# Performance work log

Measured on AMD Instinct MI355X. Metric: run time of the kernel, lower is better.

## Reference

```python
import jax, jax.numpy as jnp
import numpy as np

B, S, D = 32, 512, 512          # batch, max splits, HIDDEN_SIZE
H2 = D // 2                      # bidirectional GRU hidden per direction = 256
HEADS = 8
ATT_H = 512                      # ML_ATT_HIDDEN
DK = ATT_H // HEADS
LN_EPS = 1e-5


def setup_inputs() -> dict:
    key = jax.random.key(0)
    ks = jax.random.split(key, 20)
    n = lambda k, shp, s=0.05: jax.random.normal(k, shp, dtype=jnp.float32) * s
    lengths = jax.random.randint(ks[0], (B,), 1, S + 1)
    masks = (jnp.arange(S)[None, :] < lengths[:, None]).astype(jnp.int32)
    return {
        "splits": n(ks[1], (B, S, D), 1.0),
        "w_ih_f": n(ks[2], (3 * H2, D)), "w_hh_f": n(ks[3], (3 * H2, H2)),
        "b_ih_f": n(ks[4], (3 * H2,)), "b_hh_f": n(ks[5], (3 * H2,)),
        "w_ih_b": n(ks[6], (3 * H2, D)), "w_hh_b": n(ks[7], (3 * H2, H2)),
        "b_ih_b": n(ks[8], (3 * H2,)), "b_hh_b": n(ks[9], (3 * H2,)),
        "ln1_g": jnp.ones((D,), jnp.float32), "ln1_b": jnp.zeros((D,), jnp.float32),
        "wq": n(ks[10], (ATT_H, D)), "bq": n(ks[11], (ATT_H,)),
        "wk": n(ks[12], (ATT_H, D)), "bk": n(ks[13], (ATT_H,)),
        "wv": n(ks[14], (ATT_H, D)), "bv": n(ks[15], (ATT_H,)),
        "wo": n(ks[16], (D, ATT_H)), "bo": n(ks[17], (D,)),
        "ln2_g": jnp.ones((D,), jnp.float32), "ln2_b": jnp.zeros((D,), jnp.float32),
        "lengths": lengths, "masks": masks,
    }


def _gru_dir(x, m, w_ih, w_hh, b_ih, b_hh):
    """x: (B,S,D) float, m: (B,S) float {0,1}. Masked GRU, packed-sequence semantics:
    hidden frozen past length, outputs zero at pads, returns (outputs (B,S,H2), h_final (B,H2))."""
    xg = jnp.einsum('bsd,gd->bsg', x, w_ih) + b_ih   # precompute input gates (B,S,3H2)
    xg_t = xg.transpose(1, 0, 2)                      # (S,B,3H2)
    m_t = m.T[:, :, None]                             # (S,B,1)
    h0 = jnp.zeros((x.shape[0], w_hh.shape[1]), x.dtype)

    def step(h, inp):
        xg_s, m_s = inp
        hg = h @ w_hh.T + b_hh
        xr, xz, xn = jnp.split(xg_s, 3, -1)
        hr, hz, hn = jnp.split(hg, 3, -1)
        r = jax.nn.sigmoid(xr + hr)
        z = jax.nn.sigmoid(xz + hz)
        ncand = jnp.tanh(xn + r * hn)
        h_new = (1.0 - z) * ncand + z * h
        h = m_s * h_new + (1.0 - m_s) * h
        return h, h * m_s

    hT, ys = jax.lax.scan(step, h0, (xg_t, m_t))
    return ys.transpose(1, 0, 2), hT


def _layernorm(x, g, b):
    mu = x.mean(-1, keepdims=True)
    var = ((x - mu) ** 2).mean(-1, keepdims=True)
    return (x - mu) / jnp.sqrt(var + LN_EPS) * g + b


def reference(splits, w_ih_f, w_hh_f, b_ih_f, b_hh_f, w_ih_b, w_hh_b, b_ih_b, b_hh_b,
              ln1_g, ln1_b, wq, bq, wk, bk, wv, bv, wo, bo, ln2_g, ln2_b,
              lengths, masks):
    mf = masks.astype(splits.dtype)  # (B,S)
    # bidirectional masked GRU (split_rnn)
    out_f, h_f = _gru_dir(splits, mf, w_ih_f, w_hh_f, b_ih_f, b_hh_f)
    out_b_rev, h_b = _gru_dir(splits[:, ::-1], mf[:, ::-1], w_ih_b, w_hh_b, b_ih_b, b_hh_b)
    outputs = jnp.concatenate([out_f, out_b_rev[:, ::-1]], -1)  # (B,S,D)
    hidden = jnp.concatenate([h_f, h_b], -1)                    # (B,D)
    zm = (lengths != 0).astype(outputs.dtype)
    outputs = outputs * zm[:, None, None]
    hidden = hidden * zm[:, None]
    # split_rnn_norm (LAYER_NORM_USE)
    outputs = _layernorm(outputs, ln1_g, ln1_b)
    # CONTEXT_ATT: masked multi-head self-attention
    m3 = mf[:, None, :] * mf[:, :, None]        # (B,S,S)
    bsz = outputs.shape[0]

    def proj(x, w, b):
        return (x @ w.T + b).reshape(bsz, -1, HEADS, DK).transpose(0, 2, 1, 3)

    q = proj(outputs, wq, bq)
    k = proj(outputs, wk, bk)
    v = proj(outputs, wv, bv)
    scores = jnp.einsum('bhqd,bhkd->bhqk', q, k) / np.sqrt(DK).astype(outputs.dtype)
    mask4 = m3[:, None, :, :]
    scores = jnp.where(mask4 == 0, jnp.asarray(-1e8, scores.dtype), scores)
    p = jax.nn.softmax(scores, axis=-1) * mask4
    attn = jnp.einsum('bhqk,bhkd->bhqd', p, v)
    concat = attn.transpose(0, 2, 1, 3).reshape(bsz, -1, HEADS * DK)
    o = concat @ wo.T + bo
    rowmask = (m3.sum(-1, keepdims=True) > 0).astype(o.dtype)   # (B,S,1)
    o = o * rowmask
    # residual + attn_norm
    outputs = _layernorm(outputs + o, ln2_g, ln2_b)
    return outputs, hidden
```

## Files before the change

kernel.cpp:

```cpp
#include <hip/hip_runtime.h>
#include <hip/hip_bf16.h>
#include <hip/hip_fp16.h>


typedef __bf16 bf16_t;
typedef _Float16 f16_t;
typedef __bf16 bf16x8 __attribute__((ext_vector_type(8)));
typedef __bf16 bf16x4 __attribute__((ext_vector_type(4)));
typedef _Float16 f16x8 __attribute__((ext_vector_type(8)));
typedef float f32x4 __attribute__((ext_vector_type(4)));

#define NB 32
#define NS 512
#define ND 512
#define NH 8
#define DKq 64
#define CH 32

static __device__ __forceinline__ float sigm(float x){ return 1.0f/(1.0f+__expf(-x)); }
static __device__ __forceinline__ float tanh_fast(float x){ return 1.0f - 2.0f/(__expf(2.0f*x)+1.0f); }

__global__ void cvt_f32_bf16_k(const float* __restrict__ src, bf16_t* __restrict__ dst, int n4){
    int i = blockIdx.x*256 + threadIdx.x;
    if (i < n4){
        float4 v = ((const float4*)src)[i];
        bf16x4 o; o[0]=(bf16_t)v.x; o[1]=(bf16_t)v.y; o[2]=(bf16_t)v.z; o[3]=(bf16_t)v.w;
        ((bf16x4*)dst)[i] = o;
    }
}

struct CvtSeg { const float* src; bf16_t* dst; int n4; };
struct CvtArgs { CvtSeg seg[6]; };
__global__ void cvt_multi_k(CvtArgs a){
    CvtSeg s = a.seg[blockIdx.y];
    int i = blockIdx.x*256 + threadIdx.x;
    if (i < s.n4){
        float4 v = ((const float4*)s.src)[i];
        bf16x4 o; o[0]=(bf16_t)v.x; o[1]=(bf16_t)v.y; o[2]=(bf16_t)v.z; o[3]=(bf16_t)v.w;
        ((bf16x4*)s.dst)[i] = o;
    }
}

template<int MODE>
__global__ __launch_bounds__(256,2) void gemm_k(
    const bf16_t* __restrict__ A, const bf16_t* __restrict__ W,
    const float* __restrict__ bias, void* __restrict__ out, void* __restrict__ out2,
    const int* __restrict__ masks, int N)
{
    const int lane = threadIdx.x & 63;
    const int wv = threadIdx.x >> 6;
    const int wr = wv >> 1, wc = wv & 1;
    const int nx = gridDim.x;
    int lin = blockIdx.y * nx + blockIdx.x;
    int xcd = lin & 7, idx = lin >> 3;
    int yl = idx / nx, xb = idx - yl*nx;
    int yb = xcd*16 + yl;
    const int m0 = yb*128 + wr*64;
    const int n0 = xb*128 + wc*64;
    const int r16 = lane & 15, kq = lane >> 4;
    f32x4 acc[4][4] = {};
    const bf16_t* Ap = A + (size_t)(m0 + r16)*512 + kq*8;
    const bf16_t* Wp = W + (size_t)(n0 + r16)*512 + kq*8;
    #pragma unroll
    for (int kk = 0; kk < 16; ++kk){
        bf16x8 a[4], b[4];
        #pragma unroll
        for (int i=0;i<4;++i) a[i] = *(const bf16x8*)(Ap + (size_t)i*16*512 + kk*32);
        #pragma unroll
        for (int j=0;j<4;++j) b[j] = *(const bf16x8*)(Wp + (size_t)j*16*512 + kk*32);
        #pragma unroll
        for (int i=0;i<4;++i)
            #pragma unroll
            for (int j=0;j<4;++j)
                acc[i][j] = __builtin_amdgcn_mfma_f32_16x16x32_bf16(a[i], b[j], acc[i][j], 0,0,0);
    }
    #pragma unroll
    for (int i=0;i<4;++i){
        int row_base = m0 + i*16 + kq*4;
        #pragma unroll
        for (int j=0;j<4;++j){
            int col = n0 + j*16 + r16;
            float bs = bias[col];
            #pragma unroll
            for (int r=0;r<4;++r){
                int row = row_base + r;
                float v = acc[i][j][r] + bs;
                if (MODE==0){
                    if (col < 768) ((f16_t*)out)[(size_t)row*768 + col] = (f16_t)v;
                    else           ((f16_t*)out2)[(size_t)row*768 + (col-768)] = (f16_t)v;
                } else if (MODE==1){
                    int which = col >> 9, hh = (col >> 6) & 7, d = col & 63;
                    int bb = row >> 9, s = row & 511;
                    ((bf16_t*)out)[((((size_t)which*NB + bb)*NH + hh)*NS + s)*DKq + d] = (bf16_t)v;
                } else {
                    float mrow = (float)masks[row];
                    ((float*)out)[(size_t)row*N + col] = v * mrow;
                }
            }
        }
    }
}

__global__ __launch_bounds__(512,2) void gru_scan_k(
    const f16_t* __restrict__ xg_f, const f16_t* __restrict__ xg_b,
    const float* __restrict__ whh_f, const float* __restrict__ whh_b,
    const float* __restrict__ bhh_f, const float* __restrict__ bhh_b,
    const int* __restrict__ lengths,
    f16_t* __restrict__ gout,
    float* __restrict__ hidden)
{
    const int b = blockIdx.x >> 1, dir = blockIdx.x & 1;
    const int tid = threadIdx.x, lane = tid & 63, w = tid >> 6;
    const int r16 = lane & 15, kq = lane >> 4;
    const float* whh = dir ? whh_b : whh_f;
    const float* bhh = dir ? bhh_b : bhh_f;
    const f16_t* xgd = dir ? xg_b : xg_f;
    const int len = lengths[b];

    __shared__ __align__(16) f16_t  xg_lds[2][CH][768];
    __shared__ __align__(16) bf16_t h_row[2][256];

    ((bf16_t*)h_row)[tid & 511] = (bf16_t)0.0f;

    const int t0 = dir ? (NS - len) : 0;
    const int t_end = dir ? NS : len;
    const int nch = (len + CH - 1) / CH;

    auto issue_chunk = [&](int ci, int buf){
        int base = t0 + ci*CH;
        int jmax = min(CH, t_end - base);
        int pstart = dir ? (NS - base - jmax) : base;
        const char* gp = (const char*)(xgd + ((size_t)b*NS + pstart)*768);
        char* lp = (char*)(&xg_lds[buf][0][0]);
        int bytes = jmax*1536;
        #pragma unroll
        for (int k2=0; k2<6; ++k2){
            int off = (w*6 + k2)*1024;
            if (off < bytes){
                __builtin_amdgcn_global_load_lds(
                    (const __attribute__((address_space(1))) void*)(gp + off + (size_t)lane*16),
                    (__attribute__((address_space(3))) void*)(lp + off), 16, 0, 0);
            }
        }
    };
    issue_chunk(0, 0);

    bf16x8 wf[6][8];
    #pragma unroll
    for (int tt=0; tt<6; ++tt){
        int g = tt >> 1, u = tt & 1;
        int n0 = g*256 + 32*w + u*16;
        const float* wp = whh + (size_t)(n0 + r16)*256 + kq*8;
        #pragma unroll
        for (int kk=0; kk<8; ++kk){
            float4 v0 = *(const float4*)(wp + kk*32);
            float4 v1 = *(const float4*)(wp + kk*32 + 4);
            bf16x8 f;
            f[0]=(bf16_t)v0.x; f[1]=(bf16_t)v0.y; f[2]=(bf16_t)v0.z; f[3]=(bf16_t)v0.w;
            f[4]=(bf16_t)v1.x; f[5]=(bf16_t)v1.y; f[6]=(bf16_t)v1.z; f[7]=(bf16_t)v1.w;
            wf[tt][kk] = f;
        }
    }
    float bhr[2], bhz[2], bhn[2], hreg[2];
    #pragma unroll
    for (int u=0; u<2; ++u){
        int gi = 32*w + 16*u + r16;
        bhr[u] = bhh[gi]; bhz[u] = bhh[256+gi]; bhn[u] = bhh[512+gi];
        hreg[u] = 0.0f;
    }

    int hp = 0;
    for (int ci = 0; ci < nch; ++ci){
        const int cur = ci & 1;
        const int base = t0 + ci*CH;
        const int jmax = min(CH, t_end - base);
        __syncthreads();
        if (ci + 1 < nch) issue_chunk(ci+1, cur^1);
        for (int j = 0; j < jmax; ++j){
            const int xrow = dir ? (jmax-1-j) : j;
            float xr[2], xz[2], xn[2];
            if (lane < 16){
                #pragma unroll
                for (int u=0; u<2; ++u){
                    int gi = 32*w + 16*u + r16;
                    xr[u] = (float)xg_lds[cur][xrow][gi];
                    xz[u] = (float)xg_lds[cur][xrow][256+gi];
                    xn[u] = (float)xg_lds[cur][xrow][512+gi];
                }
            }
            f32x4 acc[6] = {};
            #pragma unroll
            for (int kk=0; kk<8; ++kk){
                bf16x8 a = {};
                if (r16 == 0) a = *(const bf16x8*)(&h_row[hp][kk*32 + kq*8]);
                #pragma unroll
                for (int tt=0; tt<6; ++tt)
                    acc[tt] = __builtin_amdgcn_mfma_f32_16x16x32_bf16(a, wf[tt][kk], acc[tt], 0,0,0);
            }
            if (lane < 16){
                int t = base + j;
                int pos = dir ? (NS-1-t) : t;
                #pragma unroll
                for (int u=0; u<2; ++u){
                    int gi = 32*w + 16*u + r16;
                    float hr = acc[u][0]   + bhr[u];
                    float hz = acc[2+u][0] + bhz[u];
                    float hn = acc[4+u][0] + bhn[u];
                    float rr = sigm(xr[u] + hr);
                    float z2 = sigm(xz[u] + hz);
                    float nc = tanh_fast(xn[u] + rr*hn);
                    hreg[u] = (1.0f - z2)*nc + z2*hreg[u];
                    h_row[hp^1][gi] = (bf16_t)hreg[u];
                    gout[((size_t)b*NS + pos)*512 + dir*256 + gi] = (f16_t)hreg[u];
                }
            }
            hp ^= 1;
            asm volatile("s_waitcnt lgkmcnt(0)" ::: "memory");
            __builtin_amdgcn_s_barrier();
            asm volatile("" ::: "memory");
        }
    }
    if (lane < 16){
        #pragma unroll
        for (int u=0; u<2; ++u)
            hidden[(size_t)b*512 + dir*256 + 32*w + 16*u + r16] = hreg[u];
    }
}

template<int PASS>
__global__ __launch_bounds__(256,4) void ln_k(
    const void* __restrict__ src1, const float* __restrict__ src2,
    const float* __restrict__ gg, const float* __restrict__ bb,
    void* __restrict__ dst)
{
    int row = blockIdx.x*4 + (threadIdx.x>>6);
    int lane = threadIdx.x & 63;
    int c0 = lane*8;
    float x[8];
    if (PASS==1){
        f16x8 v = *(const f16x8*)((const f16_t*)src1 + (size_t)row*512 + c0);
        #pragma unroll
        for (int i=0;i<8;++i) x[i] = (float)v[i];
    } else {
        bf16x8 v = *(const bf16x8*)((const bf16_t*)src1 + (size_t)row*512 + c0);
        const float* q = src2 + (size_t)row*512 + c0;
        float4 q0 = *(const float4*)q, q1 = *(const float4*)(q+4);
        x[0]=(float)v[0]+q0.x; x[1]=(float)v[1]+q0.y; x[2]=(float)v[2]+q0.z; x[3]=(float)v[3]+q0.w;
        x[4]=(float)v[4]+q1.x; x[5]=(float)v[5]+q1.y; x[6]=(float)v[6]+q1.z; x[7]=(float)v[7]+q1.w;
    }
    float s=0.f, sq=0.f;
    #pragma unroll
    for (int i=0;i<8;++i){ s += x[i]; sq += x[i]*x[i]; }
    #pragma unroll
    for (int m=1; m<64; m<<=1){ s += __shfl_xor(s, m, 64); sq += __shfl_xor(sq, m, 64); }
    float mu = s * (1.0f/512.0f);
    float var = sq * (1.0f/512.0f) - mu*mu;
    float rs = rsqrtf(var + 1e-5f);
    if (PASS==1){
        bf16x8 o;
        #pragma unroll
        for (int i=0;i<8;++i) o[i] = (bf16_t)((x[i]-mu)*rs*gg[c0+i] + bb[c0+i]);
        *(bf16x8*)((bf16_t*)dst + (size_t)row*512 + c0) = o;
    } else {
        float y[8];
        #pragma unroll
        for (int i=0;i<8;++i) y[i] = (x[i]-mu)*rs*gg[c0+i] + bb[c0+i];
        float* dp = (float*)dst + (size_t)row*512 + c0;
        *(float4*)dp     = make_float4(y[0],y[1],y[2],y[3]);
        *(float4*)(dp+4) = make_float4(y[4],y[5],y[6],y[7]);
    }
}

__global__ __launch_bounds__(256,2) void attn_k(
    const bf16_t* __restrict__ qkv,
    const int* __restrict__ lengths,
    bf16_t* __restrict__ concat)
{
    int lin = blockIdx.x + 8*(blockIdx.y + 8*blockIdx.z);
    int xcd = lin & 7, idx = lin >> 3;
    int qb = idx & 7;
    int bh = (xcd << 5) | (idx >> 3);
    int hh = bh & 7, b = bh >> 3;
    const int tid = threadIdx.x, lane = tid & 63, w = tid >> 6;
    const int r16 = lane & 15, kq = lane >> 4;
    const int len = lengths[b];
    const size_t bhof = ((size_t)b*NH + hh)*NS*DKq;
    const bf16_t* Q = qkv + bhof;
    const bf16_t* K = qkv + (size_t)NB*NH*NS*DKq + bhof;
    const bf16_t* V = qkv + 2*(size_t)NB*NH*NS*DKq + bhof;

    __shared__ __align__(16) bf16_t VT[32][520];
    __shared__ __align__(16) bf16_t P[4][16][40];

    const int q0 = qb*64 + w*16;
    bf16x8 aq[2];
    #pragma unroll
    for (int kk=0; kk<2; ++kk)
        aq[kk] = *(const bf16x8*)(Q + (size_t)(q0+r16)*DKq + kk*32 + kq*8);

    f32x4 sc[32] = {};
    #pragma unroll
    for (int t=0;t<32;++t){
        #pragma unroll
        for (int kk=0;kk<2;++kk){
            bf16x8 bk = *(const bf16x8*)(K + (size_t)(t*16+r16)*DKq + kk*32 + kq*8);
            sc[t] = __builtin_amdgcn_mfma_f32_16x16x32_bf16(aq[kk], bk, sc[t], 0,0,0);
        }
    }
    float mx[4] = {-3e38f,-3e38f,-3e38f,-3e38f};
    #pragma unroll
    for (int t=0;t<32;++t){
        bool valid = (t*16 + r16) < len;
        #pragma unroll
        for (int r=0;r<4;++r){
            float sv = valid ? sc[t][r]*0.125f : -3e38f;
            sc[t][r] = sv;
            mx[r] = fmaxf(mx[r], sv);
        }
    }
    #pragma unroll
    for (int m=1;m<16;m<<=1)
        #pragma unroll
        for (int r=0;r<4;++r) mx[r] = fmaxf(mx[r], __shfl_xor(mx[r], m, 64));
    float sm[4] = {0.f,0.f,0.f,0.f};
    #pragma unroll
    for (int t=0;t<32;++t){
        bool valid = (t*16 + r16) < len;
        #pragma unroll
        for (int r=0;r<4;++r){
            float p = valid ? __expf(sc[t][r] - mx[r]) : 0.0f;
            sc[t][r] = p;
            sm[r] += p;
        }
    }
    #pragma unroll
    for (int m=1;m<16;m<<=1)
        #pragma unroll
        for (int r=0;r<4;++r) sm[r] += __shfl_xor(sm[r], m, 64);
    float rs[4];
    #pragma unroll
    for (int r=0;r<4;++r) rs[r] = sm[r] > 0.f ? 1.0f/sm[r] : 0.0f;

    f32x4 ao[4] = {};
    #pragma unroll
    for (int half=0; half<2; ++half){
        __syncthreads();
        #pragma unroll
        for (int rr=0; rr<2; ++rr){
            int s = tid*2 + rr;
            const bf16_t* vp = V + (size_t)s*DKq + half*32;
            bf16x8 v0 = *(const bf16x8*)(vp);
            bf16x8 v1 = *(const bf16x8*)(vp+8);
            bf16x8 v2 = *(const bf16x8*)(vp+16);
            bf16x8 v3 = *(const bf16x8*)(vp+24);
            #pragma unroll
            for (int d=0; d<8; ++d){
                VT[d][s]=v0[d]; VT[8+d][s]=v1[d]; VT[16+d][s]=v2[d]; VT[24+d][s]=v3[d];
            }
        }
        __syncthreads();
        #pragma unroll
        for (int c=0;c<16;++c){
            #pragma unroll
            for (int tt=0;tt<2;++tt)
                #pragma unroll
                for (int r=0;r<4;++r)
                    P[w][kq*4 + r][tt*16 + r16] = (bf16_t)(sc[2*c+tt][r] * rs[r]);
            bf16x8 pa = *(const bf16x8*)(&P[w][r16][kq*8]);
            #pragma unroll
            for (int jt=0;jt<2;++jt){
                bf16x8 bvv = *(const bf16x8*)(&VT[jt*16 + r16][c*32 + kq*8]);
                ao[half*2+jt] = __builtin_amdgcn_mfma_f32_16x16x32_bf16(pa, bvv, ao[half*2+jt], 0,0,0);
            }
        }
    }
    #pragma unroll
    for (int ht=0; ht<4; ++ht){
        int d = (ht>>1)*32 + ((ht&1)*16) + r16;
        #pragma unroll
        for (int r=0;r<4;++r){
            int s = q0 + kq*4 + r;
            float v = (s < len) ? ao[ht][r] : 0.0f;
            concat[((size_t)b*NS + s)*512 + hh*DKq + d] = (bf16_t)v;
        }
    }
}

extern "C" void kernel_launch(void* const* d_in, const int* in_sizes, int n_in,
                              void* d_out, int out_size, void* d_ws, size_t ws_size,
                              hipStream_t stream){
    (void)in_sizes; (void)n_in; (void)out_size; (void)ws_size;
    const float* splits = (const float*)d_in[0];
    const float* w_ih_f = (const float*)d_in[1];
    const float* w_hh_f = (const float*)d_in[2];
    const float* b_ih_f = (const float*)d_in[3];
    const float* b_hh_f = (const float*)d_in[4];
    const float* w_ih_b = (const float*)d_in[5];
    const float* w_hh_b = (const float*)d_in[6];
    const float* b_ih_b = (const float*)d_in[7];
    const float* b_hh_b = (const float*)d_in[8];
    const float* ln1_g  = (const float*)d_in[9];
    const float* ln1_b  = (const float*)d_in[10];
    const float* wq     = (const float*)d_in[11];
    const float* bq     = (const float*)d_in[12];
    const float* wk     = (const float*)d_in[13];
    const float* bk_    = (const float*)d_in[14];
    const float* wv     = (const float*)d_in[15];
    const float* bv     = (const float*)d_in[16];
    const float* wo     = (const float*)d_in[17];
    const float* bo     = (const float*)d_in[18];
    const float* ln2_g  = (const float*)d_in[19];
    const float* ln2_b  = (const float*)d_in[20];
    const int* lengths  = (const int*)d_in[21];
    const int* masks    = (const int*)d_in[22];

    char* ws = (char*)d_ws;
    bf16_t* splits16 = (bf16_t*)(ws);
    f16_t*  xg_f     = (f16_t*)(ws + ((size_t)16<<20));
    f16_t*  xg_b     = (f16_t*)(ws + ((size_t)40<<20));
    f16_t*  gout     = (f16_t*)(ws + ((size_t)64<<20));
    bf16_t* ln1out   = (bf16_t*)(ws + ((size_t)80<<20));
    bf16_t* wih16    = (bf16_t*)(ws + ((size_t)96<<20));
    bf16_t* wqkv16   = (bf16_t*)(ws + ((size_t)98<<20));
    bf16_t* wo16     = (bf16_t*)(ws + ((size_t)100<<20));
    float*  bih      = (float*)(ws + ((size_t)101<<20));
    float*  bqkv     = (float*)(ws + ((size_t)101<<20) + 8192);
    bf16_t* qkv      = (bf16_t*)xg_f;
    float*  obuf     = (float*)xg_f;
    bf16_t* concat   = (bf16_t*)splits16;

    float* out_f = (float*)d_out;
    float* hid   = out_f + (size_t)NB*NS*ND;

    hipLaunchKernelGGL(cvt_f32_bf16_k, dim3(8192), dim3(256), 0, stream, splits, splits16, 2097152);
    CvtArgs ca;
    ca.seg[0] = { w_ih_f, wih16,          98304 };
    ca.seg[1] = { w_ih_b, wih16+393216,   98304 };
    ca.seg[2] = { wq,     wqkv16,         65536 };
    ca.seg[3] = { wk,     wqkv16+262144,  65536 };
    ca.seg[4] = { wv,     wqkv16+524288,  65536 };
    ca.seg[5] = { wo,     wo16,           65536 };
    hipLaunchKernelGGL(cvt_multi_k, dim3(384,6), dim3(256), 0, stream, ca);
    hipMemcpyAsync(bih,       b_ih_f, 768*4, hipMemcpyDeviceToDevice, stream);
    hipMemcpyAsync(bih+768,   b_ih_b, 768*4, hipMemcpyDeviceToDevice, stream);
    hipMemcpyAsync(bqkv,      bq,     512*4, hipMemcpyDeviceToDevice, stream);
    hipMemcpyAsync(bqkv+512,  bk_,    512*4, hipMemcpyDeviceToDevice, stream);
    hipMemcpyAsync(bqkv+1024, bv,     512*4, hipMemcpyDeviceToDevice, stream);
    hipMemsetAsync(gout, 0, (size_t)16<<20, stream);

    hipLaunchKernelGGL((gemm_k<0>), dim3(12,128), dim3(256), 0, stream,
                       splits16, wih16, bih, (void*)xg_f, (void*)xg_b, nullptr, 1536);
    hipLaunchKernelGGL(gru_scan_k, dim3(64), dim3(512), 0, stream,
                       xg_f, xg_b, w_hh_f, w_hh_b, b_hh_f, b_hh_b, lengths, gout, hid);
    hipLaunchKernelGGL((ln_k<1>), dim3(4096), dim3(256), 0, stream,
                       (const void*)gout, nullptr, ln1_g, ln1_b, (void*)ln1out);
    hipLaunchKernelGGL((gemm_k<1>), dim3(12,128), dim3(256), 0, stream,
                       ln1out, wqkv16, bqkv, (void*)qkv, nullptr, nullptr, 0);
    hipLaunchKernelGGL(attn_k, dim3(8,8,32), dim3(256), 0, stream, qkv, lengths, concat);
    hipLaunchKernelGGL((gemm_k<2>), dim3(4,128), dim3(256), 0, stream,
                       concat, wo16, bo, (void*)obuf, nullptr, masks, 512);
    hipLaunchKernelGGL((ln_k<2>), dim3(4096), dim3(256), 0, stream,
                       (const void*)ln1out, obuf, ln2_g, ln2_b, (void*)out_f);
}
```

Baseline: 1.249 ms.

## Replace GRU recurrent MFMA with fp16 dot2 across 1024 threads, batch output stores

The GRU scan kernel drops the MFMA matvec, which wasted most of its lanes because only one row of the A operand was non-zero. In its place, each of 1024 threads computes partial dot products with packed fp16 fdot2 on register-resident weights, and the partials are reduced with cross-lane shuffles. Hidden outputs are staged in LDS per chunk and written to global memory as coalesced vector stores, and the chunk size is halved to fit the larger block. The recurrent weights and hidden state change from bf16 to fp16, and the per-step barrier becomes a full __syncthreads across 16 waves, which may cost more synchronization per step.

Result: slower. 1.298 ms (+3.9%).

```diff
diff --git a/kernel.cpp b/kernel.cpp
--- a/kernel.cpp
+++ b/kernel.cpp
@@ -8,6 +8,8 @@
 typedef __bf16 bf16x8 __attribute__((ext_vector_type(8)));
 typedef __bf16 bf16x4 __attribute__((ext_vector_type(4)));
 typedef _Float16 f16x8 __attribute__((ext_vector_type(8)));
+typedef _Float16 f16x4 __attribute__((ext_vector_type(4)));
+typedef _Float16 f16x2 __attribute__((ext_vector_type(2)));
 typedef float f32x4 __attribute__((ext_vector_type(4)));
 
 #define NB 32
@@ -15,7 +17,7 @@
 #define ND 512
 #define NH 8
 #define DKq 64
-#define CH 32
+#define CH 16
 
 static __device__ __forceinline__ float sigm(float x){ return 1.0f/(1.0f+__expf(-x)); }
 static __device__ __forceinline__ float tanh_fast(float x){ return 1.0f - 2.0f/(__expf(2.0f*x)+1.0f); }
@@ -101,7 +103,7 @@
     }
 }
 
-__global__ __launch_bounds__(512,2) void gru_scan_k(
+__global__ __launch_bounds__(1024,4) void gru_scan_k(
     const f16_t* __restrict__ xg_f, const f16_t* __restrict__ xg_b,
     const float* __restrict__ whh_f, const float* __restrict__ whh_b,
     const float* __restrict__ bhh_f, const float* __restrict__ bhh_b,
@@ -112,15 +114,17 @@
     const int b = blockIdx.x >> 1, dir = blockIdx.x & 1;
     const int tid = threadIdx.x, lane = tid & 63, w = tid >> 6;
     const int r16 = lane & 15, kq = lane >> 4;
+    const int c = (w << 4) | r16;
     const float* whh = dir ? whh_b : whh_f;
     const float* bhh = dir ? bhh_b : bhh_f;
     const f16_t* xgd = dir ? xg_b : xg_f;
     const int len = lengths[b];
 
-    __shared__ __align__(16) f16_t  xg_lds[2][CH][768];
-    __shared__ __align__(16) bf16_t h_row[2][256];
-
-    ((bf16_t*)h_row)[tid & 511] = (bf16_t)0.0f;
+    __shared__ __align__(16) f16_t xg_lds[2][CH][768];
+    __shared__ __align__(16) f16_t go_lds[CH][256];
+    __shared__ __align__(16) f16_t h_row[2][256];
+
+    if (tid < 512) ((f16_t*)h_row)[tid] = (f16_t)0.0f;
 
     const int t0 = dir ? (NS - len) : 0;
     const int t_end = dir ? NS : len;
@@ -134,40 +138,33 @@
         char* lp = (char*)(&xg_lds[buf][0][0]);
         int bytes = jmax*1536;
         #pragma unroll
-        for (int k2=0; k2<6; ++k2){
-            int off = (w*6 + k2)*1024;
-            if (off < bytes){
+        for (int k2=0; k2<2; ++k2){
+            int woff = (k2*16 + w)*1024;
+            if (woff < bytes){
                 __builtin_amdgcn_global_load_lds(
-                    (const __attribute__((address_space(1))) void*)(gp + off + (size_t)lane*16),
-                    (__attribute__((address_space(3))) void*)(lp + off), 16, 0, 0);
+                    (const __attribute__((address_space(1))) void*)(gp + woff + (size_t)lane*16),
+                    (__attribute__((address_space(3))) void*)(lp + woff), 16, 0, 0);
             }
         }
     };
     issue_chunk(0, 0);
 
-    bf16x8 wf[6][8];
-    #pragma unroll
-    for (int tt=0; tt<6; ++tt){
-        int g = tt >> 1, u = tt & 1;
-        int n0 = g*256 + 32*w + u*16;
-        const float* wp = whh + (size_t)(n0 + r16)*256 + kq*8;
+    f16x2 wd[3][8][4];
+    #pragma unroll
+    for (int g=0; g<3; ++g){
+        const float* wp = whh + (size_t)(g*256 + c)*256 + kq*8;
         #pragma unroll
         for (int kk=0; kk<8; ++kk){
             float4 v0 = *(const float4*)(wp + kk*32);
             float4 v1 = *(const float4*)(wp + kk*32 + 4);
-            bf16x8 f;
-            f[0]=(bf16_t)v0.x; f[1]=(bf16_t)v0.y; f[2]=(bf16_t)v0.z; f[3]=(bf16_t)v0.w;
-            f[4]=(bf16_t)v1.x; f[5]=(bf16_t)v1.y; f[6]=(bf16_t)v1.z; f[7]=(bf16_t)v1.w;
-            wf[tt][kk] = f;
-        }
-    }
-    float bhr[2], bhz[2], bhn[2], hreg[2];
-    #pragma unroll
-    for (int u=0; u<2; ++u){
-        int gi = 32*w + 16*u + r16;
-        bhr[u] = bhh[gi]; bhz[u] = bhh[256+gi]; bhn[u] = bhh[512+gi];
-        hreg[u] = 0.0f;
-    }
+            wd[g][kk][0] = (f16x2){(f16_t)v0.x, (f16_t)v0.y};
+            wd[g][kk][1] = (f16x2){(f16_t)v0.z, (f16_t)v0.w};
+            wd[g][kk][2] = (f16x2){(f16_t)v1.x, (f16_t)v1.y};
+            wd[g][kk][3] = (f16x2){(f16_t)v1.z, (f16_t)v1.w};
+        }
+    }
+    const float bhr = bhh[c], bhz = bhh[256+c], bhn = bhh[512+c];
+    float hreg = 0.0f;
 
     int hp = 0;
     for (int ci = 0; ci < nch; ++ci){
@@ -178,53 +175,47 @@
         if (ci + 1 < nch) issue_chunk(ci+1, cur^1);
         for (int j = 0; j < jmax; ++j){
             const int xrow = dir ? (jmax-1-j) : j;
-            float xr[2], xz[2], xn[2];
+            float a0 = 0.f, a1 = 0.f, a2 = 0.f;
+            #pragma unroll
+            for (int kk=0; kk<8; ++kk){
+                f16x8 hv = *(const f16x8*)(&h_row[hp][kk*32 + kq*8]);
+                #pragma unroll
+                for (int e=0; e<4; ++e){
+                    f16x2 h2 = {hv[2*e], hv[2*e+1]};
+                    a0 = __builtin_amdgcn_fdot2(wd[0][kk][e], h2, a0, false);
+                    a1 = __builtin_amdgcn_fdot2(wd[1][kk][e], h2, a1, false);
+                    a2 = __builtin_amdgcn_fdot2(wd[2][kk][e], h2, a2, false);
+                }
+            }
+            a0 += __shfl_xor(a0, 16); a0 += __shfl_xor(a0, 32);
+            a1 += __shfl_xor(a1, 16); a1 += __shfl_xor(a1, 32);
+            a2 += __shfl_xor(a2, 16); a2 += __shfl_xor(a2, 32);
             if (lane < 16){
-                #pragma unroll
-                for (int u=0; u<2; ++u){
-                    int gi = 32*w + 16*u + r16;
-                    xr[u] = (float)xg_lds[cur][xrow][gi];
-                    xz[u] = (float)xg_lds[cur][xrow][256+gi];
-                    xn[u] = (float)xg_lds[cur][xrow][512+gi];
-                }
-            }
-            f32x4 acc[6] = {};
-            #pragma unroll
-            for (int kk=0; kk<8; ++kk){
-                bf16x8 a = {};
-                if (r16 == 0) a = *(const bf16x8*)(&h_row[hp][kk*32 + kq*8]);
-                #pragma unroll
-                for (int tt=0; tt<6; ++tt)
-                    acc[tt] = __builtin_amdgcn_mfma_f32_16x16x32_bf16(a, wf[tt][kk], acc[tt], 0,0,0);
-            }
-            if (lane < 16){
-                int t = base + j;
-                int pos = dir ? (NS-1-t) : t;
-                #pragma unroll
-                for (int u=0; u<2; ++u){
-                    int gi = 32*w + 16*u + r16;
-                    float hr = acc[u][0]   + bhr[u];
-                    float hz = acc[2+u][0] + bhz[u];
-                    float hn = acc[4+u][0] + bhn[u];
-                    float rr = sigm(xr[u] + hr);
-                    float z2 = sigm(xz[u] + hz);
-                    float nc = tanh_fast(xn[u] + rr*hn);
-                    hreg[u] = (1.0f - z2)*nc + z2*hreg[u];
-                    h_row[hp^1][gi] = (bf16_t)hreg[u];
-                    gout[((size_t)b*NS + pos)*512 + dir*256 + gi] = (f16_t)hreg[u];
-                }
+                float hr = a0 + bhr;
+                float hz = a1 + bhz;
+                float hn = a2 + bhn;
+                float xr = (float)xg_lds[cur][xrow][c];
+                float xz = (float)xg_lds[cur][xrow][256+c];
+                float xn = (float)xg_lds[cur][xrow][512+c];
+                float rr = sigm(xr + hr);
+                float z2 = sigm(xz + hz);
+                float nc = tanh_fast(xn + rr*hn);
+                hreg = (1.0f - z2)*nc + z2*hreg;
+                h_row[hp^1][c] = (f16_t)hreg;
+                go_lds[j][c]   = (f16_t)hreg;
             }
             hp ^= 1;
-            asm volatile("s_waitcnt lgkmcnt(0)" ::: "memory");
-            __builtin_amdgcn_s_barrier();
-            asm volatile("" ::: "memory");
-        }
-    }
-    if (lane < 16){
-        #pragma unroll
-        for (int u=0; u<2; ++u)
-            hidden[(size_t)b*512 + dir*256 + 32*w + 16*u + r16] = hreg[u];
-    }
+            __syncthreads();
+        }
+        if (w < jmax){
+            int t = base + w;
+            int pos = dir ? (NS-1-t) : t;
+            f16x4 vv = *(const f16x4*)(&go_lds[w][lane*4]);
+            *(f16x4*)(gout + ((size_t)b*NS + pos)*512 + dir*256 + lane*4) = vv;
+        }
+    }
+    if (lane < 16)
+        hidden[(size_t)b*512 + dir*256 + c] = hreg;
 }
 
 template<int PASS>
@@ -360,16 +351,16 @@
         }
         __syncthreads();
         #pragma unroll
-        for (int c=0;c<16;++c){
+        for (int cI=0;cI<16;++cI){
             #pragma unroll
             for (int tt=0;tt<2;++tt)
                 #pragma unroll
                 for (int r=0;r<4;++r)
-                    P[w][kq*4 + r][tt*16 + r16] = (bf16_t)(sc[2*c+tt][r] * rs[r]);
+                    P[w][kq*4 + r][tt*16 + r16] = (bf16_t)(sc[2*cI+tt][r] * rs[r]);
             bf16x8 pa = *(const bf16x8*)(&P[w][r16][kq*8]);
             #pragma unroll
             for (int jt=0;jt<2;++jt){
-                bf16x8 bvv = *(const bf16x8*)(&VT[jt*16 + r16][c*32 + kq*8]);
+                bf16x8 bvv = *(const bf16x8*)(&VT[jt*16 + r16][cI*32 + kq*8]);
                 ao[half*2+jt] = __builtin_amdgcn_mfma_f32_16x16x32_bf16(pa, bvv, ao[half*2+jt], 0,0,0);
             }
         }
@@ -450,7 +441,7 @@
 
     hipLaunchKernelGGL((gemm_k<0>), dim3(12,128), dim3(256), 0, stream,
                        splits16, wih16, bih, (void*)xg_f, (void*)xg_b, nullptr, 1536);
-    hipLaunchKernelGGL(gru_scan_k, dim3(64), dim3(512), 0, stream,
+    hipLaunchKernelGGL(gru_scan_k, dim3(64), dim3(1024), 0, stream,
                        xg_f, xg_b, w_hh_f, w_hh_b, b_hh_f, b_hh_b, lengths, gout, hid);
     hipLaunchKernelGGL((ln_k<1>), dim3(4096), dim3(256), 0, stream,
                        (const void*)gout, nullptr, ln1_g, ln1_b, (void*)ln1out);
```
